# Kernel tuning notes

Measured on AMD Instinct MI355X. Metric: run time of the kernel, lower is better.

Reference implementation:

```python
import jax, jax.numpy as jnp
import numpy as np

GROUP = 64       # quantization block size along in_features
SCALING = 2.0    # delta_alpha / r = 32 / 16


def setup_inputs() -> dict:
    key = jax.random.key(0)
    k1, k2, k3, k4 = jax.random.split(key, 4)
    B, S, D_IN, D_OUT = 8, 2048, 4096, 4096
    x = jax.random.normal(k1, (B, S, D_IN), dtype=jnp.float32)
    # int4 codes in [0, 16); symmetric zero-point 8
    w_codes = jax.random.randint(k2, (D_OUT, D_IN), 0, 16, dtype=jnp.int32)
    # per-(row, group) scales; small positive values like bnb absmax/7
    scales = jax.random.uniform(k3, (D_OUT, D_IN // GROUP), dtype=jnp.float32) * 0.02
    base_bias = jax.random.normal(k4, (D_OUT,), dtype=jnp.float32)
    delta_w = jax.random.normal(jax.random.fold_in(key, 5), (D_OUT, D_IN), dtype=jnp.float32) * 0.01
    return {"x": x, "w_codes": w_codes, "scales": scales,
            "base_bias": base_bias, "delta_w": delta_w}


def _dequant(w_codes, scales):
    # symmetric int4 dequant: w = (code - 8) * scale_of_its_group
    d_out, d_in = w_codes.shape
    w = (w_codes.astype(scales.dtype) - 8.0).reshape(d_out, d_in // GROUP, GROUP)
    w = w * scales[:, :, None]
    return w.reshape(d_out, d_in)


def reference(x, w_codes, scales, base_bias, delta_w):
    # base layer: int4 dequant-matmul + bias
    w = _dequant(w_codes, scales)                       # [D_out, D_in]
    base = jnp.einsum("bsi,oi->bso", x, w) + base_bias  # [B, S, D_out]
    # delta branch: dropout(p=0) -> matmul -> scale -> residual add
    delta = jnp.einsum("bsi,oi->bso", x, delta_w) * SCALING
    return base + delta
```

## Files before the change

### kernel.cpp

```cpp
#include <hip/hip_runtime.h>
#include <cstdint>

#define D_IN   4096
#define D_OUT  4096
#define MTOT   16384
#define SCALING 2.0f

#define BM 256
#define BN 256
#define BK 64
#define KT (D_IN / BK)

typedef float  f32x4  __attribute__((ext_vector_type(4)));
typedef __bf16 bf16x8 __attribute__((ext_vector_type(8)));
typedef unsigned short ushort8 __attribute__((ext_vector_type(8)));
typedef int    int4v  __attribute__((ext_vector_type(4)));
typedef float  float4v __attribute__((ext_vector_type(4)));

__device__ __forceinline__ unsigned short f2bf(float f) {
  union { float f; unsigned u; } v; v.f = f;
  unsigned r = v.u + 0x7FFF + ((v.u >> 16) & 1);
  return (unsigned short)(r >> 16);
}

#define ASYNC16(g, l)                                                        \
  __builtin_amdgcn_global_load_lds(                                          \
      (const __attribute__((address_space(1))) unsigned int*)(g),            \
      (__attribute__((address_space(3))) unsigned int*)(l), 16, 0, 0)

#define BAR    __builtin_amdgcn_s_barrier()
#define VMW(n) asm volatile("s_waitcnt vmcnt(" #n ")" ::: "memory")

__global__ __launch_bounds__(256) void prep_x_kernel(const float* __restrict__ x,
                                                     unsigned short* __restrict__ xbf) {
  int i = (blockIdx.x * 256 + threadIdx.x) * 8;
  float4v lo = *(const float4v*)(x + i);
  float4v hi = *(const float4v*)(x + i + 4);
  ushort8 o;
  o[0] = f2bf(lo[0]); o[1] = f2bf(lo[1]); o[2] = f2bf(lo[2]); o[3] = f2bf(lo[3]);
  o[4] = f2bf(hi[0]); o[5] = f2bf(hi[1]); o[6] = f2bf(hi[2]); o[7] = f2bf(hi[3]);
  *(ushort8*)(xbf + i) = o;
}

__global__ __launch_bounds__(256) void prep_w_kernel(const int* __restrict__ codes,
                                                     const float* __restrict__ scales,
                                                     const float* __restrict__ delta,
                                                     unsigned short* __restrict__ weff) {
  int i = (blockIdx.x * 256 + threadIdx.x) * 8;
  int row = i >> 12;
  int col = i & (D_IN - 1);
  float s = scales[(row << 6) + (col >> 6)];
  int4v   c0 = *(const int4v*)(codes + i);
  int4v   c1 = *(const int4v*)(codes + i + 4);
  float4v d0 = *(const float4v*)(delta + i);
  float4v d1 = *(const float4v*)(delta + i + 4);
  ushort8 o;
  o[0] = f2bf((float)(c0[0] - 8) * s + SCALING * d0[0]);
  o[1] = f2bf((float)(c0[1] - 8) * s + SCALING * d0[1]);
  o[2] = f2bf((float)(c0[2] - 8) * s + SCALING * d0[2]);
  o[3] = f2bf((float)(c0[3] - 8) * s + SCALING * d0[3]);
  o[4] = f2bf((float)(c1[0] - 8) * s + SCALING * d1[0]);
  o[5] = f2bf((float)(c1[1] - 8) * s + SCALING * d1[1]);
  o[6] = f2bf((float)(c1[2] - 8) * s + SCALING * d1[2]);
  o[7] = f2bf((float)(c1[3] - 8) * s + SCALING * d1[3]);
  *(ushort8*)(weff + i) = o;
}


#define STAGE_A(buf_, kt_, h_) do {                                          \
    char* d_ = &lds[buf_][h_][0] + tid * 16;                                 \
    const unsigned short* s_ = gA + (size_t)(h_) * 128 * D_IN + (kt_) * 64;  \
    ASYNC16(s_, d_);                                                         \
    ASYNC16(s_ + 64 * D_IN, d_ + 8192);                                      \
  } while (0)

#define STAGE_B(buf_, kt_, h_) do {                                          \
    char* d_ = &lds[buf_][2 + (h_)][0] + tid * 16;                           \
    const unsigned short* s_ = gB + (size_t)(h_) * 128 * D_IN + (kt_) * 64;  \
    ASYNC16(s_, d_);                                                         \
    ASYNC16(s_ + 64 * D_IN, d_ + 8192);                                      \
  } while (0)

#define RD_A(buf_, h_) do {                                                  \
    _Pragma("unroll")                                                        \
    for (int m2 = 0; m2 < 4; ++m2) {                                         \
      const char* p_ = &lds[buf_][wr][0] + ((h_)*4 + m2) * 2048 + rowb;      \
      A[m2][0] = *(const bf16x8*)(p_ + koff0);                               \
      A[m2][1] = *(const bf16x8*)(p_ + koff1);                               \
    } } while (0)

#define RD_B(buf_, h_, dst_) do {                                            \
    _Pragma("unroll")                                                        \
    for (int n2 = 0; n2 < 2; ++n2) {                                         \
      const char* p_ = &lds[buf_][2 + (wc >> 1)][0] + (wc & 1) * 8192 +      \
                       (h_) * 4096 + n2 * 2048 + rowb;                       \
      dst_[n2][0] = *(const bf16x8*)(p_ + koff0);                            \
      dst_[n2][1] = *(const bf16x8*)(p_ + koff1);                            \
    } } while (0)

#define MM16(bfr_, mh_, nh_) do {                                            \
    __builtin_amdgcn_s_setprio(1);                                           \
    _Pragma("unroll")                                                        \
    for (int m2 = 0; m2 < 4; ++m2) {                                         \
      _Pragma("unroll")                                                      \
      for (int n2 = 0; n2 < 2; ++n2) {                                       \
        acc[(mh_)*4 + m2][(nh_)*2 + n2] = __builtin_amdgcn_mfma_f32_16x16x32_bf16( \
            A[m2][0], bfr_[n2][0], acc[(mh_)*4 + m2][(nh_)*2 + n2], 0, 0, 0);      \
        acc[(mh_)*4 + m2][(nh_)*2 + n2] = __builtin_amdgcn_mfma_f32_16x16x32_bf16( \
            A[m2][1], bfr_[n2][1], acc[(mh_)*4 + m2][(nh_)*2 + n2], 0, 0, 0);      \
      } }                                                                    \
    __builtin_amdgcn_s_setprio(0);                                           \
  } while (0)

#define KTILE(buf_, g_, SA_, SB_, VM_) do {                                  \
                                                                     \
    if (SA_) STAGE_A((buf_) ^ 1, (g_) + 1, 0);                               \
    BAR;                                                                     \
    RD_A(buf_, 0);                                                           \
    RD_B(buf_, 0, B0);                                                       \
    MM16(B0, 0, 0);                                                          \
                                                                     \
    if (SA_) STAGE_A((buf_) ^ 1, (g_) + 1, 1);                               \
    BAR;                                                                     \
    RD_B(buf_, 1, B1);                                                       \
    MM16(B1, 0, 1);                                                          \
                                                                     \
    if (SB_) STAGE_B(buf_, (g_) + 2, 0);                                     \
    BAR;                                                                     \
    RD_A(buf_, 1);                                                           \
    MM16(B0, 1, 0);                                                          \
                                                                     \
    if (SB_) STAGE_B(buf_, (g_) + 2, 1);                                     \
    BAR;                                                                     \
    MM16(B1, 1, 1);                                                          \
    VM_;                                                                     \
  } while (0)

__global__ __launch_bounds__(512, 2) void gemm8_kernel(const unsigned short* __restrict__ xbf,
                                                       const unsigned short* __restrict__ weff,
                                                       const float* __restrict__ bias,
                                                       float* __restrict__ out) {
  __shared__ __attribute__((aligned(1024))) char lds[2][4][16384];

  const int tid  = threadIdx.x;
  const int lane = tid & 63;
  const int wid  = tid >> 6;
  const int wr   = wid >> 2;
  const int wc   = wid & 3;

  const int id  = blockIdx.x;
  const int nid = (id & 7) * 128 + (id >> 3);
  const int tn  = nid & 15;
  const int tm  = nid >> 4;

  const int rowb  = (lane & 15) * 128;
  const int kx    = (lane & 7) << 4;
  const int koff0 = (((lane >> 4) * 16) ^ kx);
  const int koff1 = ((64 + (lane >> 4) * 16) ^ kx);

  const int sr = tid >> 3;
  const int ke = ((tid & 7) ^ (sr & 7)) * 8;
  const unsigned short* gA = xbf  + (size_t)(tm * BM + sr) * D_IN + ke;
  const unsigned short* gB = weff + (size_t)(tn * BN + sr) * D_IN + ke;

  f32x4 acc[8][4] = {};
  bf16x8 A[4][2], B0[2][2], B1[2][2];

  STAGE_A(0, 0, 0); STAGE_A(0, 0, 1);
  STAGE_B(0, 0, 0); STAGE_B(0, 0, 1);
  STAGE_B(1, 1, 0); STAGE_B(1, 1, 1);
  VMW(4);

  for (int g = 0; g < KT - 2; g += 2) {
    KTILE(0, g,     1, 1, VMW(4));
    KTILE(1, g + 1, 1, 1, VMW(4));
  }
  KTILE(0, KT - 2, 1, 0, VMW(0));
  KTILE(1, KT - 1, 0, 0, (void)0);

  const int row0 = tm * BM + wr * 128 + (lane >> 4) * 4;
  const int col0 = tn * BN + wc * 64 + (lane & 15);
#pragma unroll
  for (int n = 0; n < 4; ++n) {
    const int col = col0 + n * 16;
    const float bv = bias[col];
#pragma unroll
    for (int m = 0; m < 8; ++m) {
      const int r = row0 + m * 16;
#pragma unroll
      for (int j = 0; j < 4; ++j)
        out[(size_t)(r + j) * D_OUT + col] = acc[m][n][j] + bv;
    }
  }
}

extern "C" void kernel_launch(void* const* d_in, const int* in_sizes, int n_in,
                              void* d_out, int out_size, void* d_ws, size_t ws_size,
                              hipStream_t stream) {
  const float* x      = (const float*)d_in[0];
  const int*   codes  = (const int*)d_in[1];
  const float* scales = (const float*)d_in[2];
  const float* bias   = (const float*)d_in[3];
  const float* delta  = (const float*)d_in[4];
  float* out = (float*)d_out;

  unsigned short* xbf  = (unsigned short*)d_ws;
  unsigned short* weff = xbf + (size_t)MTOT * D_IN;

  prep_x_kernel<<<(MTOT * D_IN) / (256 * 8), 256, 0, stream>>>(x, xbf);
  prep_w_kernel<<<(D_OUT * D_IN) / (256 * 8), 256, 0, stream>>>(codes, scales, delta, weff);

  gemm8_kernel<<<(MTOT / BM) * (D_OUT / BN), 512, 0, stream>>>(xbf, weff, bias, out);
}
```

Baseline: 556.4 us.

## Restructure GEMM k-loop to two barriers per tile with simple double buffering

Replaces the staggered four-phase k-tile schedule (A staged one tile ahead, B two tiles ahead, four barriers per tile) with a plain double-buffer scheme. The next tile's B is issued at the start and its A mid-tile, with two barriers per k-tile. Both B halves are read from LDS up front. The aim is to cut barrier and sync overhead, at the cost of a shorter prefetch distance for B and more registers live at once.

```diff
diff --git a/kernel.cpp b/kernel.cpp
--- a/kernel.cpp
+++ b/kernel.cpp
@@ -67,18 +67,22 @@
 }
 
 
-#define STAGE_A(buf_, kt_, h_) do {                                          \
-    char* d_ = &lds[buf_][h_][0] + tid * 16;                                 \
-    const unsigned short* s_ = gA + (size_t)(h_) * 128 * D_IN + (kt_) * 64;  \
+#define STAGE_A(buf_, kt_) do {                                              \
+    char* d_ = &lds[buf_][0][0] + tid * 16;                                  \
+    const unsigned short* s_ = gA + (size_t)(kt_) * 64;                      \
     ASYNC16(s_, d_);                                                         \
-    ASYNC16(s_ + 64 * D_IN, d_ + 8192);                                      \
-  } while (0)
-
-#define STAGE_B(buf_, kt_, h_) do {                                          \
-    char* d_ = &lds[buf_][2 + (h_)][0] + tid * 16;                           \
-    const unsigned short* s_ = gB + (size_t)(h_) * 128 * D_IN + (kt_) * 64;  \
+    ASYNC16(s_ +  64 * D_IN, d_ + 8192);                                     \
+    ASYNC16(s_ + 128 * D_IN, d_ + 16384);                                    \
+    ASYNC16(s_ + 192 * D_IN, d_ + 24576);                                    \
+  } while (0)
+
+#define STAGE_B(buf_, kt_) do {                                              \
+    char* d_ = &lds[buf_][2][0] + tid * 16;                                  \
+    const unsigned short* s_ = gB + (size_t)(kt_) * 64;                      \
     ASYNC16(s_, d_);                                                         \
-    ASYNC16(s_ + 64 * D_IN, d_ + 8192);                                      \
+    ASYNC16(s_ +  64 * D_IN, d_ + 8192);                                     \
+    ASYNC16(s_ + 128 * D_IN, d_ + 16384);                                    \
+    ASYNC16(s_ + 192 * D_IN, d_ + 24576);                                    \
   } while (0)
 
 #define RD_A(buf_, h_) do {                                                  \
@@ -112,28 +116,22 @@
     __builtin_amdgcn_s_setprio(0);                                           \
   } while (0)
 
-#define KTILE(buf_, g_, SA_, SB_, VM_) do {                                  \
-                                                                     \
-    if (SA_) STAGE_A((buf_) ^ 1, (g_) + 1, 0);                               \
+#define KTILE(buf_, g_, SB_, SA_, VM_) do {                                  \
+                                                                    \
+    if (SB_) STAGE_B((buf_) ^ 1, (g_) + 1);                                  \
+    VM_;                                                                     \
     BAR;                                                                     \
     RD_A(buf_, 0);                                                           \
     RD_B(buf_, 0, B0);                                                       \
+    RD_B(buf_, 1, B1);                                                       \
     MM16(B0, 0, 0);                                                          \
-                                                                     \
-    if (SA_) STAGE_A((buf_) ^ 1, (g_) + 1, 1);                               \
-    BAR;                                                                     \
-    RD_B(buf_, 1, B1);                                                       \
     MM16(B1, 0, 1);                                                          \
-                                                                     \
-    if (SB_) STAGE_B(buf_, (g_) + 2, 0);                                     \
+                                                                    \
+    if (SA_) STAGE_A((buf_) ^ 1, (g_) + 1);                                  \
     BAR;                                                                     \
     RD_A(buf_, 1);                                                           \
     MM16(B0, 1, 0);                                                          \
-                                                                     \
-    if (SB_) STAGE_B(buf_, (g_) + 2, 1);                                     \
-    BAR;                                                                     \
     MM16(B1, 1, 1);                                                          \
-    VM_;                                                                     \
   } while (0)
 
 __global__ __launch_bounds__(512, 2) void gemm8_kernel(const unsigned short* __restrict__ xbf,
@@ -166,17 +164,15 @@
   f32x4 acc[8][4] = {};
   bf16x8 A[4][2], B0[2][2], B1[2][2];
 
-  STAGE_A(0, 0, 0); STAGE_A(0, 0, 1);
-  STAGE_B(0, 0, 0); STAGE_B(0, 0, 1);
-  STAGE_B(1, 1, 0); STAGE_B(1, 1, 1);
-  VMW(4);
+  STAGE_A(0, 0);
+  STAGE_B(0, 0);
 
   for (int g = 0; g < KT - 2; g += 2) {
     KTILE(0, g,     1, 1, VMW(4));
     KTILE(1, g + 1, 1, 1, VMW(4));
   }
-  KTILE(0, KT - 2, 1, 0, VMW(0));
-  KTILE(1, KT - 1, 0, 0, (void)0);
+  KTILE(0, KT - 2, 1, 1, VMW(4));
+  KTILE(1, KT - 1, 0, 0, VMW(0));
 
   const int row0 = tm * BM + wr * 128 + (lane >> 4) * 4;
   const int col0 = tn * BN + wc * 64 + (lane & 15);
```

New measurement: 576.9 us. 3.7% more time.
